# Kernel tuning notes

Hardware: AMD Instinct MI355X
Metric: run time of the kernel (lower is better)

## Reference

```python
import jax, jax.numpy as jnp
import numpy as np

B, E, D_IN, D_OUT = 4, 262144, 64, 64
NUM_SEG = 10000  # = index.max()+1 by construction (fill_max)


def setup_inputs() -> dict:
    key = jax.random.key(0)
    ks = jax.random.split(key, 12)
    s_in = 1.0 / np.sqrt(D_IN)
    s_cat = 1.0 / np.sqrt(4 * D_IN)
    inp = {
        "index": jax.random.randint(ks[0], (B, E, 2), 0, NUM_SEG, dtype=jnp.int64)
        if jax.config.jax_enable_x64 else jax.random.randint(ks[0], (B, E, 2), 0, NUM_SEG, dtype=jnp.int32),
        "value": jax.random.normal(ks[1], (B, E, D_IN), dtype=jnp.float32),
        "W_self": jax.random.uniform(ks[2], (D_IN, D_IN), jnp.float32, -s_in, s_in),
        "b_self": jax.random.uniform(ks[3], (D_IN,), jnp.float32, -s_in, s_in),
        "W_row": jax.random.uniform(ks[4], (D_IN, D_IN), jnp.float32, -s_in, s_in),
        "b_row": jax.random.uniform(ks[5], (D_IN,), jnp.float32, -s_in, s_in),
        "W_col": jax.random.uniform(ks[6], (D_IN, D_IN), jnp.float32, -s_in, s_in),
        "b_col": jax.random.uniform(ks[7], (D_IN,), jnp.float32, -s_in, s_in),
        "W_glob": jax.random.uniform(ks[8], (D_IN, D_IN), jnp.float32, -s_in, s_in),
        "b_glob": jax.random.uniform(ks[9], (D_IN,), jnp.float32, -s_in, s_in),
        "W_out": jax.random.uniform(ks[10], (D_OUT, 4 * D_IN), jnp.float32, -s_cat, s_cat),
        "b_out": jax.random.uniform(ks[11], (D_OUT,), jnp.float32, -s_cat, s_cat),
    }
    return inp


def _sparse_mean(idx, val):
    # idx: [B, E] int, val: [B, E, D]. Per-batch segment mean, gathered back to edges.
    def one(i, v):
        seg = jax.ops.segment_sum(v, i, num_segments=NUM_SEG)            # [NUM_SEG, D]
        cnt = jax.ops.segment_sum(jnp.ones(i.shape, v.dtype), i, num_segments=NUM_SEG) + 1e-9
        return (seg / cnt[:, None])[i]                                    # expand back: [E, D]
    return jax.vmap(one)(idx, val)


def _lin(x, W, b):
    return jnp.einsum('bed,od->beo', x, W) + b


def reference(index, value, W_self, b_self, W_row, b_row, W_col, b_col,
              W_glob, b_glob, W_out, b_out):
    row_mean = _sparse_mean(index[:, :, 0], value)                        # [B, E, D]
    col_mean = _sparse_mean(index[:, :, 1], value)                        # [B, E, D]
    glob = jnp.mean(value, axis=1)                                        # [B, D]
    glob = (glob @ W_glob.T + b_glob)[:, None, :]                         # [B, 1, D] -> broadcast
    glob = jnp.broadcast_to(glob, value.shape)
    stacked = jnp.concatenate([
        _lin(value, W_self, b_self),
        _lin(row_mean, W_row, b_row),
        _lin(col_mean, W_col, b_col),
        glob,
    ], axis=2)                                                            # [B, E, 4D]
    out = jax.nn.leaky_relu(_lin(stacked, W_out, b_out), negative_slope=0.01)
    return (index, out)
```

## Files before the change

kernel.cpp:

```cpp
#include <hip/hip_runtime.h>


#define BB 4
#define EE 262144
#define DD 64
#define NSEG 10000
#define CAP 64

#define OFF_MT_SELF 0
#define OFF_MT_ROW  4096
#define OFF_MT_COL  8192
#define OFF_MT_GLOB 12288
#define OFF_CONSTB  16384
#define OFF_GSUM    16640
#define OFF_TROW    16896
#define OFF_TCOL    2576896
#define OFF_CNT     5136896
#define ZERO_BEG    16640
#define ZERO_END    5216896
#define OFF_LIST    5216896
#define OFF_GPART   10336896
#define WS_END      10976896

__device__ __forceinline__ void aadd(float* p, float v) {
#if defined(__HIP_DEVICE_COMPILE__)
    unsafeAtomicAdd(p, v);
#else
    (void)p; (void)v;
#endif
}

__global__ __launch_bounds__(256) void k_cvtidx(const int* __restrict__ index,
                                                float* __restrict__ outf) {
    long i = ((long)blockIdx.x * 256 + threadIdx.x) * 4;
    int4 v = *(const int4*)(index + i);
    *(float4*)(outf + i) = make_float4((float)v.x, (float)v.y, (float)v.z, (float)v.w);
}

__global__ __launch_bounds__(256) void k_prep(const float* __restrict__ W_out,
        const float* __restrict__ W_self, const float* __restrict__ W_row,
        const float* __restrict__ W_col,  const float* __restrict__ W_glob,
        float* __restrict__ ws) {
    int m  = blockIdx.x >> 4;
    int ob = (blockIdx.x & 15) * 4;
    int d  = threadIdx.x & 63;
    int o  = ob + (threadIdx.x >> 6);
    const float* W = (m == 0) ? W_self : (m == 1) ? W_row : (m == 2) ? W_col : W_glob;
    float* MT = ws + ((m == 0) ? OFF_MT_SELF : (m == 1) ? OFF_MT_ROW : (m == 2) ? OFF_MT_COL : OFF_MT_GLOB);
    float acc = 0.f;
    #pragma unroll
    for (int k = 0; k < 64; ++k)
        acc += W_out[o * 256 + m * 64 + k] * W[k * 64 + d];
    MT[d * 64 + o] = acc;
}


__global__ __launch_bounds__(256) void k_fill(const int* __restrict__ index,
                                              float* __restrict__ ws) {
    int b = blockIdx.x & 3;
    int e = (blockIdx.x >> 2) * 256 + threadIdx.x;
    long be = (long)b * EE + e;
    int2 idx = *(const int2*)(index + be * 2);
    int* cnt  = (int*)(ws + OFF_CNT);
    int* list = (int*)(ws + OFF_LIST);
    int pr = atomicAdd(&cnt[(0 * BB + b) * NSEG + idx.x], 1);
    if (pr < CAP) list[((long)(0 * BB + b) * NSEG + idx.x) * CAP + pr] = e;
    int pc = atomicAdd(&cnt[(1 * BB + b) * NSEG + idx.y], 1);
    if (pc < CAP) list[((long)(1 * BB + b) * NSEG + idx.y) * CAP + pc] = e;
}

__global__ __launch_bounds__(256) void k_segsum(const float* __restrict__ value,
                                                float* __restrict__ ws) {
    __shared__ float smt[4096];
    __shared__ float red[4][64];
    int t  = blockIdx.x / NSEG;
    int j  = blockIdx.x % NSEG;
    int b  = j / 2500, jj = j % 2500;
    int wid = threadIdx.x >> 6, lane = threadIdx.x & 63;
    int s  = jj * 4 + wid;
    for (int i = threadIdx.x; i < 4096; i += 256)
        smt[i] = ws[(t ? OFF_MT_COL : OFF_MT_ROW) + i];
    __syncthreads();

    int n = ((const int*)(ws + OFF_CNT))[(t * BB + b) * NSEG + s];
    const int* list = (const int*)(ws + OFF_LIST) + ((long)(t * BB + b) * NSEG + s) * CAP;
    int m = n < CAP ? n : CAP;
    int e_l = (lane < m) ? list[lane] : 0;
    const float* vb = value + (long)b * EE * 64;
    float sum = 0.f;
    for (int i = 0; i < m; i += 8) {
        #pragma unroll
        for (int k = 0; k < 8; ++k) {
            int ek = __shfl(e_l, i + k);
            float vk = vb[(long)ek * 64 + lane];
            sum += (i + k < m) ? vk : 0.f;
        }
    }
    red[wid][lane] = sum;
    __syncthreads();
    if (t == 0 && wid == 0)
        ws[OFF_GPART + ((long)b * 2500 + jj) * 64 + lane] =
            red[0][lane] + red[1][lane] + red[2][lane] + red[3][lane];

    float mean = sum / ((float)n + 1e-9f);
    float acc = 0.f;
    #pragma unroll
    for (int d = 0; d < 64; ++d)
        acc += __shfl(mean, d) * smt[d * 64 + lane];
    ws[(t ? OFF_TCOL : OFF_TROW) + ((long)b * NSEG + s) * 64 + lane] = acc;
}

__global__ __launch_bounds__(256) void k_gsum_csr(float* __restrict__ ws) {
    int b = blockIdx.x / 10, chunk = blockIdx.x % 10;
    int d = threadIdx.x & 63, part = threadIdx.x >> 6;
    int base = chunk * 250;
    float acc = 0.f;
    for (int r = base + part; r < base + 250; r += 4)
        acc += ws[OFF_GPART + ((long)b * 2500 + r) * 64 + d];
    __shared__ float red[256];
    red[threadIdx.x] = acc;
    __syncthreads();
    if (threadIdx.x < 64)
        aadd(ws + OFF_GSUM + b * 64 + threadIdx.x,
             red[threadIdx.x] + red[64 + threadIdx.x] + red[128 + threadIdx.x] + red[192 + threadIdx.x]);
}


__global__ __launch_bounds__(256) void k_scatter_f(const int* __restrict__ index,
        const float* __restrict__ value, float* __restrict__ ws) {
    int b = blockIdx.x & 3;
    long e = (long)(blockIdx.x >> 2) * 256 + threadIdx.x;
    long be = (long)b * EE + e;
    int2 idx = *(const int2*)(index + be * 2);
    const float4* v4 = (const float4*)(value + be * 64);
    float* srow = ws + OFF_TROW + ((long)b * NSEG + idx.x) * 64;
    float* scol = ws + OFF_TCOL + ((long)b * NSEG + idx.y) * 64;
    #pragma unroll
    for (int i = 0; i < 16; ++i) {
        float4 v = v4[i];
        aadd(srow + i * 4 + 0, v.x); aadd(srow + i * 4 + 1, v.y);
        aadd(srow + i * 4 + 2, v.z); aadd(srow + i * 4 + 3, v.w);
        aadd(scol + i * 4 + 0, v.x); aadd(scol + i * 4 + 1, v.y);
        aadd(scol + i * 4 + 2, v.z); aadd(scol + i * 4 + 3, v.w);
    }
    aadd(ws + OFF_CNT + (0 * BB + b) * NSEG + idx.x, 1.f);
    aadd(ws + OFF_CNT + (1 * BB + b) * NSEG + idx.y, 1.f);
}

__global__ __launch_bounds__(256) void k_gsum_f(float* __restrict__ ws) {
    int b = blockIdx.x / 40, chunk = blockIdx.x % 40;
    int d = threadIdx.x & 63, part = threadIdx.x >> 6;
    const float* seg = ws + OFF_TROW + (long)b * NSEG * 64;
    int base = chunk * 250;
    float acc = 0.f;
    for (int s = base + part; s < base + 250; s += 4)
        acc += seg[s * 64 + d];
    __shared__ float red[256];
    red[threadIdx.x] = acc;
    __syncthreads();
    if (threadIdx.x < 64)
        aadd(ws + OFF_GSUM + b * 64 + threadIdx.x,
             red[threadIdx.x] + red[64 + threadIdx.x] + red[128 + threadIdx.x] + red[192 + threadIdx.x]);
}

__global__ __launch_bounds__(256) void k_seg_xform_f(float* __restrict__ ws) {
    __shared__ float smt[2][4096];
    for (int i = threadIdx.x; i < 4096; i += 256) {
        smt[0][i] = ws[OFF_MT_ROW + i];
        smt[1][i] = ws[OFF_MT_COL + i];
    }
    __syncthreads();
    int wid = threadIdx.x >> 6, lane = threadIdx.x & 63;
    long sg = (long)blockIdx.x * 4 + wid;
    int t = sg >= (long)BB * NSEG;
    long r = sg - (long)t * BB * NSEG;
    int b = (int)(r / NSEG), s = (int)(r % NSEG);
    float* buf = ws + (t ? OFF_TCOL : OFF_TROW) + ((long)b * NSEG + s) * 64;
    float cnt = ws[OFF_CNT + (t * BB + b) * NSEG + s];
    float mean = buf[lane] / (cnt + 1e-9f);
    const float* MT = smt[t];
    float acc = 0.f;
    #pragma unroll
    for (int d = 0; d < 64; ++d)
        acc += __shfl(mean, d) * MT[d * 64 + lane];
    buf[lane] = acc;
}


__global__ __launch_bounds__(256) void k_constb(const float* __restrict__ W_out,
        const float* __restrict__ b_self, const float* __restrict__ b_row,
        const float* __restrict__ b_col,  const float* __restrict__ b_glob,
        const float* __restrict__ b_out,  float* __restrict__ ws) {
    int o = threadIdx.x;
    if (o >= 64) return;
    float cv = b_out[o];
    #pragma unroll
    for (int k = 0; k < 64; ++k) {
        cv += W_out[o * 256 +       k] * b_self[k]
            + W_out[o * 256 +  64 + k] * b_row[k]
            + W_out[o * 256 + 128 + k] * b_col[k]
            + W_out[o * 256 + 192 + k] * b_glob[k];
    }
    const float invE = 1.f / (float)EE;
    for (int b = 0; b < BB; ++b) {
        float g = cv;
        #pragma unroll
        for (int d = 0; d < 64; ++d)
            g += ws[OFF_MT_GLOB + d * 64 + o] * (ws[OFF_GSUM + b * 64 + d] * invE);
        ws[OFF_CONSTB + b * 64 + o] = g;
    }
}

__global__ __launch_bounds__(256) void k_main(const int* __restrict__ index,
        const float* __restrict__ value, const float* __restrict__ ws,
        float* __restrict__ out) {
    __shared__ float4 smt[64][16];
    __shared__ float4 scb[16];
    int b = blockIdx.x & 3;
    for (int i = threadIdx.x; i < 1024; i += 256)
        smt[i >> 4][i & 15] = ((const float4*)(ws + OFF_MT_SELF))[i];
    if (threadIdx.x < 16)
        scb[threadIdx.x] = ((const float4*)(ws + OFF_CONSTB + b * 64))[threadIdx.x];
    __syncthreads();

    long e  = (long)(blockIdx.x >> 2) * 256 + threadIdx.x;
    long be = (long)b * EE + e;
    int2 idx = *(const int2*)(index + be * 2);
    const float4* tr = (const float4*)(ws + OFF_TROW + ((long)b * NSEG + idx.x) * 64);
    const float4* tc = (const float4*)(ws + OFF_TCOL + ((long)b * NSEG + idx.y) * 64);

    float4 acc[16];
    #pragma unroll
    for (int i = 0; i < 16; ++i) {
        float4 a = tr[i], c = tc[i];
        acc[i].x = a.x + c.x; acc[i].y = a.y + c.y;
        acc[i].z = a.z + c.z; acc[i].w = a.w + c.w;
    }

    const float4* v4 = (const float4*)(value + be * 64);
    #pragma unroll
    for (int dc = 0; dc < 16; ++dc) {
        float4 vv = v4[dc];
        int db = dc * 4;
        #pragma unroll
        for (int o = 0; o < 16; ++o) { float4 m = smt[db + 0][o];
            acc[o].x += vv.x * m.x; acc[o].y += vv.x * m.y; acc[o].z += vv.x * m.z; acc[o].w += vv.x * m.w; }
        #pragma unroll
        for (int o = 0; o < 16; ++o) { float4 m = smt[db + 1][o];
            acc[o].x += vv.y * m.x; acc[o].y += vv.y * m.y; acc[o].z += vv.y * m.z; acc[o].w += vv.y * m.w; }
        #pragma unroll
        for (int o = 0; o < 16; ++o) { float4 m = smt[db + 2][o];
            acc[o].x += vv.z * m.x; acc[o].y += vv.z * m.y; acc[o].z += vv.z * m.z; acc[o].w += vv.z * m.w; }
        #pragma unroll
        for (int o = 0; o < 16; ++o) { float4 m = smt[db + 3][o];
            acc[o].x += vv.w * m.x; acc[o].y += vv.w * m.y; acc[o].z += vv.w * m.z; acc[o].w += vv.w * m.w; }
    }

    float4* op = (float4*)(out + be * 64);
    #pragma unroll
    for (int i = 0; i < 16; ++i) {
        float4 a = acc[i], k = scb[i];
        a.x += k.x; a.y += k.y; a.z += k.z; a.w += k.w;
        a.x = a.x >= 0.f ? a.x : 0.01f * a.x;
        a.y = a.y >= 0.f ? a.y : 0.01f * a.y;
        a.z = a.z >= 0.f ? a.z : 0.01f * a.z;
        a.w = a.w >= 0.f ? a.w : 0.01f * a.w;
        op[i] = a;
    }
}

extern "C" void kernel_launch(void* const* d_in, const int* in_sizes, int n_in,
                              void* d_out, int out_size, void* d_ws, size_t ws_size,
                              hipStream_t stream) {
    const int*   index  = (const int*)  d_in[0];
    const float* value  = (const float*)d_in[1];
    const float* W_self = (const float*)d_in[2];
    const float* b_self = (const float*)d_in[3];
    const float* W_row  = (const float*)d_in[4];
    const float* b_row  = (const float*)d_in[5];
    const float* W_col  = (const float*)d_in[6];
    const float* b_col  = (const float*)d_in[7];
    const float* W_glob = (const float*)d_in[8];
    const float* b_glob = (const float*)d_in[9];
    const float* W_out  = (const float*)d_in[10];
    const float* b_out  = (const float*)d_in[11];
    float* ws = (float*)d_ws;

    float* outf = (float*)d_out;
    float* out  = outf + (size_t)BB * EE * 2;

    k_cvtidx<<<BB * EE * 2 / 1024, 256, 0, stream>>>(index, outf);
    hipMemsetAsync(ws + ZERO_BEG, 0, (size_t)(ZERO_END - ZERO_BEG) * sizeof(float), stream);
    k_prep<<<64, 256, 0, stream>>>(W_out, W_self, W_row, W_col, W_glob, ws);

    if (ws_size >= (size_t)WS_END * sizeof(float)) {
        k_fill<<<BB * (EE / 256), 256, 0, stream>>>(index, ws);
        k_segsum<<<2 * NSEG, 256, 0, stream>>>(value, ws);
        k_gsum_csr<<<BB * 10, 256, 0, stream>>>(ws);
    } else {
        k_scatter_f<<<BB * (EE / 256), 256, 0, stream>>>(index, value, ws);
        k_gsum_f<<<BB * 40, 256, 0, stream>>>(ws);
        k_seg_xform_f<<<2 * BB * NSEG / 4, 256, 0, stream>>>(ws);
    }

    k_constb<<<1, 256, 0, stream>>>(W_out, b_self, b_row, b_col, b_glob, b_out, ws);
    k_main<<<BB * (EE / 256), 256, 0, stream>>>(index, value, ws, out);
}
```

Before: 957.7 us.

## Split each edge's 64 outputs across four threads in main kernel

The main per-edge kernel now assigns four threads to each edge, each computing 16 of the 64 output channels, instead of one thread computing all 64. This cuts per-thread accumulator registers from 64 to 16, which should raise occupancy. The gather, output writes and weight reads become more coalesced across neighbouring threads. In exchange, each thread now reloads the full 64-float value row, so value reads are repeated four times (mostly served from cache), and the grid has four times as many blocks.

```diff
diff --git a/kernel.cpp b/kernel.cpp
--- a/kernel.cpp
+++ b/kernel.cpp
@@ -223,49 +223,48 @@
         scb[threadIdx.x] = ((const float4*)(ws + OFF_CONSTB + b * 64))[threadIdx.x];
     __syncthreads();
 
-    long e  = (long)(blockIdx.x >> 2) * 256 + threadIdx.x;
+    int el = threadIdx.x >> 2;
+    int q  = threadIdx.x & 3;
+    long e  = (long)(blockIdx.x >> 2) * 64 + el;
     long be = (long)b * EE + e;
     int2 idx = *(const int2*)(index + be * 2);
     const float4* tr = (const float4*)(ws + OFF_TROW + ((long)b * NSEG + idx.x) * 64);
     const float4* tc = (const float4*)(ws + OFF_TCOL + ((long)b * NSEG + idx.y) * 64);
 
-    float4 acc[16];
-    #pragma unroll
-    for (int i = 0; i < 16; ++i) {
-        float4 a = tr[i], c = tc[i];
-        acc[i].x = a.x + c.x; acc[i].y = a.y + c.y;
-        acc[i].z = a.z + c.z; acc[i].w = a.w + c.w;
+    float4 acc[4];
+    #pragma unroll
+    for (int j = 0; j < 4; ++j) {
+        float4 a = tr[q * 4 + j], c = tc[q * 4 + j];
+        acc[j].x = a.x + c.x; acc[j].y = a.y + c.y;
+        acc[j].z = a.z + c.z; acc[j].w = a.w + c.w;
     }
 
     const float4* v4 = (const float4*)(value + be * 64);
     #pragma unroll
     for (int dc = 0; dc < 16; ++dc) {
         float4 vv = v4[dc];
-        int db = dc * 4;
         #pragma unroll
-        for (int o = 0; o < 16; ++o) { float4 m = smt[db + 0][o];
-            acc[o].x += vv.x * m.x; acc[o].y += vv.x * m.y; acc[o].z += vv.x * m.z; acc[o].w += vv.x * m.w; }
-        #pragma unroll
-        for (int o = 0; o < 16; ++o) { float4 m = smt[db + 1][o];
-            acc[o].x += vv.y * m.x; acc[o].y += vv.y * m.y; acc[o].z += vv.y * m.z; acc[o].w += vv.y * m.w; }
-        #pragma unroll
-        for (int o = 0; o < 16; ++o) { float4 m = smt[db + 2][o];
-            acc[o].x += vv.z * m.x; acc[o].y += vv.z * m.y; acc[o].z += vv.z * m.z; acc[o].w += vv.z * m.w; }
-        #pragma unroll
-        for (int o = 0; o < 16; ++o) { float4 m = smt[db + 3][o];
-            acc[o].x += vv.w * m.x; acc[o].y += vv.w * m.y; acc[o].z += vv.w * m.z; acc[o].w += vv.w * m.w; }
+        for (int c = 0; c < 4; ++c) {
+            float vc = (c == 0) ? vv.x : (c == 1) ? vv.y : (c == 2) ? vv.z : vv.w;
+            #pragma unroll
+            for (int j = 0; j < 4; ++j) {
+                float4 m = smt[dc * 4 + c][q * 4 + j];
+                acc[j].x += vc * m.x; acc[j].y += vc * m.y;
+                acc[j].z += vc * m.z; acc[j].w += vc * m.w;
+            }
+        }
     }
 
     float4* op = (float4*)(out + be * 64);
     #pragma unroll
-    for (int i = 0; i < 16; ++i) {
-        float4 a = acc[i], k = scb[i];
+    for (int j = 0; j < 4; ++j) {
+        float4 a = acc[j], k = scb[q * 4 + j];
         a.x += k.x; a.y += k.y; a.z += k.z; a.w += k.w;
         a.x = a.x >= 0.f ? a.x : 0.01f * a.x;
         a.y = a.y >= 0.f ? a.y : 0.01f * a.y;
         a.z = a.z >= 0.f ? a.z : 0.01f * a.z;
         a.w = a.w >= 0.f ? a.w : 0.01f * a.w;
-        op[i] = a;
+        op[q * 4 + j] = a;
     }
 }
 
@@ -304,5 +303,5 @@
     }
 
     k_constb<<<1, 256, 0, stream>>>(W_out, b_self, b_row, b_col, b_glob, b_out, ws);
-    k_main<<<BB * (EE / 256), 256, 0, stream>>>(index, value, ws, out);
-}
+    k_main<<<BB * (EE / 64), 256, 0, stream>>>(index, value, ws, out);
+}
```

Measured after the change: 911.6 us. -4.8%, faster.
